# Kernel tuning notes

Measured on AMD Instinct MI355X. Metric: run time of the kernel, lower is better.

Reference implementation:

```python
import jax, jax.numpy as jnp
import numpy as np

GROUPS = 9  # hardcoded in GTLModuleV1.forward


def setup_inputs() -> dict:
    key = jax.random.key(0)
    k1, k2, k3 = jax.random.split(key, 3)
    B, C, N, K = 4, 144, 16384, 16
    queryandkey = jax.random.normal(k1, (B, C, N), dtype=jnp.float32)
    value = jax.random.normal(k2, (B, C, N), dtype=jnp.float32)
    idx_knn = jax.random.randint(k3, (B, N, K), 0, N, dtype=jnp.int32)
    return {"queryandkey": queryandkey, "value": value, "idx_knn": idx_knn}


def _gather_neighbours(x, idx_flat, B, G, d, N, K):
    # x: (B, G, d, N); idx_flat: (B, 1, 1, N*K) -> (B, G, d, N, K)
    g = jnp.take_along_axis(x, jnp.broadcast_to(idx_flat, (B, G, d, N * K)), axis=3)
    return g.reshape(B, G, d, N, K)


def reference(queryandkey, value, idx_knn):
    B, C, N = queryandkey.shape
    K = idx_knn.shape[-1]
    G = GROUPS
    d = C // G  # Cl = C (Cnl = 0 in GTLModuleV1)

    q = queryandkey.reshape(B, G, d, N)          # LocalQuery == LocalKey source
    v = value.reshape(B, G, d, N)
    idx_flat = idx_knn.reshape(B, 1, 1, N * K)

    key_g = _gather_neighbours(q, idx_flat, B, G, d, N, K)  # (B,G,d,N,K)
    val_g = _gather_neighbours(v, idx_flat, B, G, d, N, K)  # (B,G,d,N,K)

    # LocalAtt = sum_d Q * K_gathered, softmax over neighbors
    att = jnp.einsum('bgdn,bgdnk->bgnk', q, key_g)
    att = jax.nn.softmax(att, axis=-1)                       # (B,G,N,K)

    # attention centrality: scatter_add of attention weights onto neighbor ids
    cent = jnp.zeros((B, G, N), dtype=att.dtype).at[
        jnp.arange(B)[:, None, None, None],
        jnp.arange(G)[None, :, None, None],
        idx_knn[:, None, :, :],
    ].add(att)                                               # (B,G,N)

    # weighted aggregation of gathered values
    feat = jnp.einsum('bgnk,bgdnk->bgdn', att, val_g).reshape(B, C, N)
    return feat, cent
```

## Files before the change

### kernel.cpp

```cpp
#include <hip/hip_runtime.h>
#include <hip/hip_fp16.h>

#define BATCH 4
#define CHAN  144
#define NPTS  16384
#define KNN   16
#define GRP   9
#define DIM   16
#define ROWU2 160
#define PCHA  16
#define PCHB  32
#define NPAIR (BATCH * GRP)

#define TT 32

typedef __attribute__((ext_vector_type(2))) _Float16 h2v;
typedef __attribute__((ext_vector_type(4))) float    f4v;
typedef __attribute__((ext_vector_type(4))) int      i4v;
typedef __attribute__((ext_vector_type(4))) unsigned u4v;
__device__ __forceinline__ h2v as_h2(unsigned int u) {
  union { unsigned int u; h2v h; } c; c.u = u; return c.h;
}
__device__ __forceinline__ float2 h2f(unsigned u) {
  union { unsigned u; __half2 h; } c; c.u = u;
  return __half22float2(c.h);
}

template<int J>
__device__ __forceinline__ int ibcast(int v) {
  return __builtin_amdgcn_update_dpp(0, v, (J) * 0x55, 0xF, 0xF, true);
}
template<int C>
__device__ __forceinline__ float fxor(float x) {
  int r = __builtin_amdgcn_update_dpp(0, __builtin_bit_cast(int, x), C, 0xF, 0xF, true);
  return __builtin_bit_cast(float, r);
}

__global__ __launch_bounds__(256) void pack_qv_kernel(
    const float* __restrict__ q, const float* __restrict__ v,
    unsigned int* __restrict__ qvT) {
  __shared__ float tq[TT][TT + 1];
  __shared__ float tv[TT][TT + 1];
  const int b = blockIdx.z;
  const float* qb = q + (size_t)b * CHAN * NPTS;
  const float* vb = v + (size_t)b * CHAN * NPTS;
  unsigned int* out = qvT + (size_t)b * NPTS * ROWU2;
  const int n0 = blockIdx.x * TT;
  const int c0 = blockIdx.y * TT;
  const int t = threadIdx.x;

  {
    const int cl = t >> 3, nq = (t & 7) * 4;
    const int c = c0 + cl;
    if (c < CHAN) {
      const float4 a = *(const float4*)&qb[(size_t)c * NPTS + n0 + nq];
      tq[cl][nq + 0] = a.x; tq[cl][nq + 1] = a.y;
      tq[cl][nq + 2] = a.z; tq[cl][nq + 3] = a.w;
      const float4 w = *(const float4*)&vb[(size_t)c * NPTS + n0 + nq];
      tv[cl][nq + 0] = w.x; tv[cl][nq + 1] = w.y;
      tv[cl][nq + 2] = w.z; tv[cl][nq + 3] = w.w;
    }
  }
  __syncthreads();
  {
    const int nl = t >> 3, cq = (t & 7) * 4;
    const int c = c0 + cq;
    if (c < CHAN) {
      __half2 k01 = __halves2half2(__float2half_rn(tq[cq + 0][nl]),
                                   __float2half_rn(tq[cq + 1][nl]));
      __half2 v01 = __halves2half2(__float2half_rn(tv[cq + 0][nl]),
                                   __float2half_rn(tv[cq + 1][nl]));
      __half2 k23 = __halves2half2(__float2half_rn(tq[cq + 2][nl]),
                                   __float2half_rn(tq[cq + 3][nl]));
      __half2 v23 = __halves2half2(__float2half_rn(tv[cq + 2][nl]),
                                   __float2half_rn(tv[cq + 3][nl]));
      *(uint4*)&out[(size_t)(n0 + nl) * ROWU2 + c] =
          make_uint4(*(unsigned int*)&k01, *(unsigned int*)&v01,
                     *(unsigned int*)&k23, *(unsigned int*)&v23);
    }
  }
}

__global__ __launch_bounds__(512, 4) void gtl_pair_kernel(
    const unsigned int* __restrict__ qvT,
    const int*   __restrict__ idx,
    float* __restrict__ feat,
    float* __restrict__ partA)
{
  const int i = blockIdx.x;
  const int x = i & 7, sblk = i >> 3;
  const int PU = x + 8 * (sblk >> 4);
  const int chunk = sblk & 15;
  const int b = PU >> 2, j = PU & 3;

  extern __shared__ float lcent[];
  const int tid = threadIdx.x;

  f4v* l4 = (f4v*)lcent;
  #pragma unroll
  for (int ii = 0; ii < 2 * NPTS / 4 / 512; ++ii)
    l4[ii * 512 + tid] = (f4v){0.f, 0.f, 0.f, 0.f};
  __syncthreads();

  const int lane = tid & 63;
  const int wv   = tid >> 6;
  const int slot = lane >> 3;
  const int e    = lane & 7;
  const int gh   = e >> 2;
  const int d    = e & 3;

  const char* qvb  = (const char*)qvT + (size_t)b * NPTS * (ROWU2 * 4);
  const char* idxB = (const char*)idx + (size_t)b * NPTS * (KNN * 4);
  const unsigned laneB  = (unsigned)(j * 128 + e * 16);
  const unsigned idxoff = (unsigned)(d * 16);

  int n = chunk * 1024 + wv * 8 + slot;
  i4v idq; u4v qq;
  asm volatile("global_load_dwordx4 %0, %1, %2"
               : "=v"(idq) : "v"((unsigned)n * 64u + idxoff), "s"(idxB));
  asm volatile("global_load_dwordx4 %0, %1, %2"
               : "=v"(qq) : "v"((unsigned)n * (ROWU2 * 4u) + laneB), "s"(qvb));
  asm volatile("s_waitcnt vmcnt(0)" ::: "memory");
  __builtin_amdgcn_sched_barrier(0);

  for (int it = 0; it < 16; ++it) {
    const h2v q01 = as_h2(qq.x);
    const h2v q23 = as_h2(qq.z);

    u4v kvA[8], kvB[8];
#define GISS(DST, K)                                                         \
    {                                                                        \
      const int mk = ibcast<((K) >> 2)>(                                     \
          ((K) & 3) == 0 ? idq.x : ((K) & 3) == 1 ? idq.y                    \
                         : ((K) & 3) == 2 ? idq.z : idq.w);                  \
      const unsigned vo = (unsigned)mk * (ROWU2 * 4u) + laneB;               \
      asm volatile("global_load_dwordx4 %0, %1, %2"                          \
                   : "=v"(DST) : "v"(vo), "s"(qvb));                         \
    }
    GISS(kvA[0], 0)  GISS(kvA[1], 1)  GISS(kvA[2], 2)  GISS(kvA[3], 3)
    GISS(kvA[4], 4)  GISS(kvA[5], 5)  GISS(kvA[6], 6)  GISS(kvA[7], 7)
    GISS(kvB[0], 8)  GISS(kvB[1], 9)  GISS(kvB[2], 10) GISS(kvB[3], 11)
    GISS(kvB[4], 12) GISS(kvB[5], 13) GISS(kvB[6], 14) GISS(kvB[7], 15)
#undef GISS

    const int itn = (it + 1 < 16) ? it + 1 : it;
    const int nn = chunk * 1024 + itn * 64 + wv * 8 + slot;
    i4v idqn; u4v qqn;
    asm volatile("global_load_dwordx4 %0, %1, %2"
                 : "=v"(idqn) : "v"((unsigned)nn * 64u + idxoff), "s"(idxB));
    asm volatile("global_load_dwordx4 %0, %1, %2"
                 : "=v"(qqn) : "v"((unsigned)nn * (ROWU2 * 4u) + laneB), "s"(qvb));

    asm volatile("s_waitcnt vmcnt(10)" ::: "memory");
    __builtin_amdgcn_sched_barrier(0);

    float kp[4] = {0.f, 0.f, 0.f, 0.f};
    float sum = 0.f, a0 = 0.f, a1 = 0.f, a2 = 0.f, a3 = 0.f;
#define CSTEP(V, K)                                                          \
    {                                                                        \
      float s = __builtin_amdgcn_fdot2(as_h2((V).x), q01, 0.f, false);       \
      s = __builtin_amdgcn_fdot2(as_h2((V).z), q23, s, false);               \
      s += fxor<0xB1>(s);                                                    \
      s += fxor<0x4E>(s);                                                    \
      const float e2 = __expf(s);                                            \
      sum += e2;                                                             \
      kp[(K) & 3] = (d == ((K) >> 2)) ? e2 : kp[(K) & 3];                    \
      const float2 v01 = h2f((V).y);                                         \
      const float2 v23 = h2f((V).w);                                         \
      a0 += e2 * v01.x; a1 += e2 * v01.y; a2 += e2 * v23.x; a3 += e2 * v23.y;\
    }
    CSTEP(kvA[0], 0)  CSTEP(kvA[1], 1)  CSTEP(kvA[2], 2)  CSTEP(kvA[3], 3)
    CSTEP(kvA[4], 4)  CSTEP(kvA[5], 5)  CSTEP(kvA[6], 6)  CSTEP(kvA[7], 7)

    asm volatile("s_waitcnt vmcnt(2)" ::: "memory");
    __builtin_amdgcn_sched_barrier(0);
    CSTEP(kvB[0], 8)  CSTEP(kvB[1], 9)  CSTEP(kvB[2], 10) CSTEP(kvB[3], 11)
    CSTEP(kvB[4], 12) CSTEP(kvB[5], 13) CSTEP(kvB[6], 14) CSTEP(kvB[7], 15)
#undef CSTEP

    const float inv = 1.f / sum;

    float* lc = lcent + gh * NPTS;
    atomicAdd(&lc[idq.x], kp[0] * inv);
    atomicAdd(&lc[idq.y], kp[1] * inv);
    atomicAdd(&lc[idq.z], kp[2] * inv);
    atomicAdd(&lc[idq.w], kp[3] * inv);

    float* fb = feat + ((size_t)b * CHAN + (2 * j + gh) * DIM + 4 * d) * NPTS + n;
    __builtin_nontemporal_store(a0 * inv, fb);
    __builtin_nontemporal_store(a1 * inv, fb + NPTS);
    __builtin_nontemporal_store(a2 * inv, fb + 2 * NPTS);
    __builtin_nontemporal_store(a3 * inv, fb + 3 * NPTS);

    asm volatile("s_waitcnt vmcnt(4)" ::: "memory");
    __builtin_amdgcn_sched_barrier(0);
    n = nn; idq = idqn; qq = qqn;
  }
  asm volatile("s_waitcnt vmcnt(0)" ::: "memory");
  __builtin_amdgcn_sched_barrier(0);

  __syncthreads();
  f4v* p4 = (f4v*)(partA + ((size_t)(PU * PCHA + chunk) * 2) * NPTS);
  #pragma unroll
  for (int i2 = 0; i2 < 2 * NPTS / 4 / 512; ++i2) {
    const int j2 = (i2 * 512 + tid + chunk * 512) & 8191;
    __builtin_nontemporal_store(l4[j2], &p4[j2]);
  }
}

__global__ __launch_bounds__(512, 4) void gtl_g8_kernel(
    const unsigned int* __restrict__ qvT,
    const int*   __restrict__ idx,
    float* __restrict__ feat,
    float* __restrict__ partB)
{
  const int i = blockIdx.x;
  const int x = i & 7, sblk = i >> 3;
  const int b = x >> 1;
  const int chunk = sblk + 16 * (x & 1);

  __shared__ float lcent[NPTS];
  const int tid = threadIdx.x;
  f4v* l4 = (f4v*)lcent;
  #pragma unroll
  for (int ii = 0; ii < NPTS / 4 / 512; ++ii)
    l4[ii * 512 + tid] = (f4v){0.f, 0.f, 0.f, 0.f};
  __syncthreads();

  const int NG = 4;
  const int gstart = chunk * NG;

  const int lane = tid & 63;
  const int wv   = tid >> 6;
  const int slot = lane >> 2;
  const int d    = lane & 3;

  const char* qvb  = (const char*)qvT + (size_t)b * NPTS * (ROWU2 * 4);
  const char* idxB = (const char*)idx + (size_t)b * NPTS * (KNN * 4);
  const unsigned laneB  = (unsigned)(8 * 64 + d * 16);
  const unsigned idxoff = (unsigned)(d * 16);

  int n = gstart * 128 + wv * 16 + slot;
  i4v idq; u4v qq;
  asm volatile("global_load_dwordx4 %0, %1, %2"
               : "=v"(idq) : "v"((unsigned)n * 64u + idxoff), "s"(idxB));
  asm volatile("global_load_dwordx4 %0, %1, %2"
               : "=v"(qq) : "v"((unsigned)n * (ROWU2 * 4u) + laneB), "s"(qvb));
  asm volatile("s_waitcnt vmcnt(0)" ::: "memory");
  __builtin_amdgcn_sched_barrier(0);

  for (int it = 0; it < NG; ++it) {
    const h2v q01 = as_h2(qq.x);
    const h2v q23 = as_h2(qq.z);

    u4v kvA[8], kvB[8];
#define GISS(DST, K)                                                         \
    {                                                                        \
      const int mk = ibcast<((K) >> 2)>(                                     \
          ((K) & 3) == 0 ? idq.x : ((K) & 3) == 1 ? idq.y                    \
                         : ((K) & 3) == 2 ? idq.z : idq.w);                  \
      const unsigned vo = (unsigned)mk * (ROWU2 * 4u) + laneB;               \
      asm volatile("global_load_dwordx4 %0, %1, %2"                          \
                   : "=v"(DST) : "v"(vo), "s"(qvb));                         \
    }
    GISS(kvA[0], 0)  GISS(kvA[1], 1)  GISS(kvA[2], 2)  GISS(kvA[3], 3)
    GISS(kvA[4], 4)  GISS(kvA[5], 5)  GISS(kvA[6], 6)  GISS(kvA[7], 7)
    GISS(kvB[0], 8)  GISS(kvB[1], 9)  GISS(kvB[2], 10) GISS(kvB[3], 11)
    GISS(kvB[4], 12) GISS(kvB[5], 13) GISS(kvB[6], 14) GISS(kvB[7], 15)
#undef GISS

    const int itn = (it + 1 < NG) ? it + 1 : it;
    const int nn = (gstart + itn) * 128 + wv * 16 + slot;
    i4v idqn; u4v qqn;
    asm volatile("global_load_dwordx4 %0, %1, %2"
                 : "=v"(idqn) : "v"((unsigned)nn * 64u + idxoff), "s"(idxB));
    asm volatile("global_load_dwordx4 %0, %1, %2"
                 : "=v"(qqn) : "v"((unsigned)nn * (ROWU2 * 4u) + laneB), "s"(qvb));

    asm volatile("s_waitcnt vmcnt(10)" ::: "memory");
    __builtin_amdgcn_sched_barrier(0);

    float kp[4] = {0.f, 0.f, 0.f, 0.f};
    float sum = 0.f, a0 = 0.f, a1 = 0.f, a2 = 0.f, a3 = 0.f;
#define CSTEP(V, K)                                                          \
    {                                                                        \
      float s = __builtin_amdgcn_fdot2(as_h2((V).x), q01, 0.f, false);       \
      s = __builtin_amdgcn_fdot2(as_h2((V).z), q23, s, false);               \
      s += fxor<0xB1>(s);                                                    \
      s += fxor<0x4E>(s);                                                    \
      const float e2 = __expf(s);                                            \
      sum += e2;                                                             \
      kp[(K) & 3] = (d == ((K) >> 2)) ? e2 : kp[(K) & 3];                    \
      const float2 v01 = h2f((V).y);                                         \
      const float2 v23 = h2f((V).w);                                         \
      a0 += e2 * v01.x; a1 += e2 * v01.y; a2 += e2 * v23.x; a3 += e2 * v23.y;\
    }
    CSTEP(kvA[0], 0)  CSTEP(kvA[1], 1)  CSTEP(kvA[2], 2)  CSTEP(kvA[3], 3)
    CSTEP(kvA[4], 4)  CSTEP(kvA[5], 5)  CSTEP(kvA[6], 6)  CSTEP(kvA[7], 7)
    asm volatile("s_waitcnt vmcnt(2)" ::: "memory");
    __builtin_amdgcn_sched_barrier(0);
    CSTEP(kvB[0], 8)  CSTEP(kvB[1], 9)  CSTEP(kvB[2], 10) CSTEP(kvB[3], 11)
    CSTEP(kvB[4], 12) CSTEP(kvB[5], 13) CSTEP(kvB[6], 14) CSTEP(kvB[7], 15)
#undef CSTEP

    const float inv = 1.f / sum;
    atomicAdd(&lcent[idq.x], kp[0] * inv);
    atomicAdd(&lcent[idq.y], kp[1] * inv);
    atomicAdd(&lcent[idq.z], kp[2] * inv);
    atomicAdd(&lcent[idq.w], kp[3] * inv);

    float* fb = feat + ((size_t)b * CHAN + 8 * DIM + 4 * d) * NPTS + n;
    __builtin_nontemporal_store(a0 * inv, fb);
    __builtin_nontemporal_store(a1 * inv, fb + NPTS);
    __builtin_nontemporal_store(a2 * inv, fb + 2 * NPTS);
    __builtin_nontemporal_store(a3 * inv, fb + 3 * NPTS);

    asm volatile("s_waitcnt vmcnt(4)" ::: "memory");
    __builtin_amdgcn_sched_barrier(0);
    n = nn; idq = idqn; qq = qqn;
  }
  asm volatile("s_waitcnt vmcnt(0)" ::: "memory");
  __builtin_amdgcn_sched_barrier(0);

  __syncthreads();
  f4v* p4 = (f4v*)(partB + (size_t)(b * PCHB + chunk) * NPTS);
  #pragma unroll
  for (int i2 = 0; i2 < NPTS / 4 / 512; ++i2) {
    const int j2 = (i2 * 512 + tid + chunk * 128) & 4095;
    __builtin_nontemporal_store(l4[j2], &p4[j2]);
  }
}

__global__ __launch_bounds__(256) void reduce_cent_kernel(
    const float* __restrict__ partA, const float* __restrict__ partB,
    float* __restrict__ cent) {
  const int t = blockIdx.x * 256 + threadIdx.x;
  const int bg = t >> 12;
  const int m4 = (t & 4095) << 2;
  const int b = bg / GRP, g = bg - b * GRP;
  f4v s = (f4v){0.f, 0.f, 0.f, 0.f};
  if (g < 8) {
    const int PU = b * 4 + (g >> 1), gh = g & 1;
    const f4v* p = (const f4v*)(partA + ((size_t)(PU * PCHA) * 2 + gh) * NPTS + m4);
    #pragma unroll
    for (int i = 0; i < PCHA; ++i)
      s += __builtin_nontemporal_load(&p[(size_t)i * 2 * (NPTS / 4)]);
  } else {
    const f4v* p = (const f4v*)(partB + (size_t)(b * PCHB) * NPTS + m4);
    #pragma unroll
    for (int i = 0; i < PCHB; ++i)
      s += __builtin_nontemporal_load(&p[(size_t)i * (NPTS / 4)]);
  }
  *(f4v*)(cent + (size_t)bg * NPTS + m4) = s;
}

extern "C" void kernel_launch(void* const* d_in, const int* in_sizes, int n_in,
                              void* d_out, int out_size, void* d_ws, size_t ws_size,
                              hipStream_t stream) {
  const float* q   = (const float*)d_in[0];
  const float* v   = (const float*)d_in[1];
  const int*   idx = (const int*)d_in[2];

  float* feat = (float*)d_out;
  float* cent = feat + (size_t)BATCH * CHAN * NPTS;

  unsigned int* qvT = (unsigned int*)d_ws;
  float* partA = (float*)(qvT + (size_t)BATCH * NPTS * ROWU2);
  float* partB = partA + (size_t)16 * PCHA * 2 * NPTS;

  dim3 tg(NPTS / TT, (CHAN + TT - 1) / TT, BATCH);
  pack_qv_kernel<<<tg, 256, 0, stream>>>(q, v, qvT);

  gtl_pair_kernel<<<256, 512, 2 * NPTS * sizeof(float), stream>>>(
      qvT, idx, feat, partA);

  gtl_g8_kernel<<<128, 512, 0, stream>>>(qvT, idx, feat, partB);

  reduce_cent_kernel<<<(NPAIR * NPTS / 4) / 256, 256, 0, stream>>>(
      partA, partB, cent);
}
```

Before: 210.2 us.

## Fuse pair and group-8 attention kernels into one 1024-thread launch

Result: faster. 199.0 us (-5.3%).

```diff
diff --git a/kernel.cpp b/kernel.cpp
--- a/kernel.cpp
+++ b/kernel.cpp
@@ -9,7 +9,7 @@
 #define DIM   16
 #define ROWU2 160
 #define PCHA  16
-#define PCHB  32
+#define PCHB  64
 #define NPAIR (BATCH * GRP)
 
 #define TT 32
@@ -81,49 +81,163 @@
   }
 }
 
-__global__ __launch_bounds__(512, 4) void gtl_pair_kernel(
+__global__ __launch_bounds__(1024, 4) void gtl_fused_kernel(
     const unsigned int* __restrict__ qvT,
     const int*   __restrict__ idx,
     float* __restrict__ feat,
-    float* __restrict__ partA)
+    float* __restrict__ partA,
+    float* __restrict__ partB)
 {
+  extern __shared__ float lcent[];
   const int i = blockIdx.x;
-  const int x = i & 7, sblk = i >> 3;
-  const int PU = x + 8 * (sblk >> 4);
-  const int chunk = sblk & 15;
-  const int b = PU >> 2, j = PU & 3;
-
-  extern __shared__ float lcent[];
   const int tid = threadIdx.x;
-
   f4v* l4 = (f4v*)lcent;
-  #pragma unroll
-  for (int ii = 0; ii < 2 * NPTS / 4 / 512; ++ii)
-    l4[ii * 512 + tid] = (f4v){0.f, 0.f, 0.f, 0.f};
-  __syncthreads();
-
-  const int lane = tid & 63;
-  const int wv   = tid >> 6;
-  const int slot = lane >> 3;
-  const int e    = lane & 7;
-  const int gh   = e >> 2;
-  const int d    = e & 3;
-
-  const char* qvb  = (const char*)qvT + (size_t)b * NPTS * (ROWU2 * 4);
-  const char* idxB = (const char*)idx + (size_t)b * NPTS * (KNN * 4);
-  const unsigned laneB  = (unsigned)(j * 128 + e * 16);
-  const unsigned idxoff = (unsigned)(d * 16);
-
-  int n = chunk * 1024 + wv * 8 + slot;
-  i4v idq; u4v qq;
-  asm volatile("global_load_dwordx4 %0, %1, %2"
-               : "=v"(idq) : "v"((unsigned)n * 64u + idxoff), "s"(idxB));
-  asm volatile("global_load_dwordx4 %0, %1, %2"
-               : "=v"(qq) : "v"((unsigned)n * (ROWU2 * 4u) + laneB), "s"(qvb));
-  asm volatile("s_waitcnt vmcnt(0)" ::: "memory");
-  __builtin_amdgcn_sched_barrier(0);
-
-  for (int it = 0; it < 16; ++it) {
+
+  if (i < 256) {
+    const int x = i & 7, sblk = i >> 3;
+    const int PU = x + 8 * (sblk >> 4);
+    const int chunk = sblk & 15;
+    const int b = PU >> 2, j = PU & 3;
+
+    #pragma unroll
+    for (int ii = 0; ii < 2 * NPTS / 4 / 1024; ++ii)
+      l4[ii * 1024 + tid] = (f4v){0.f, 0.f, 0.f, 0.f};
+    __syncthreads();
+
+    const int lane = tid & 63;
+    const int wv   = tid >> 6;
+    const int slot = lane >> 3;
+    const int e    = lane & 7;
+    const int gh   = e >> 2;
+    const int d    = e & 3;
+
+    const char* qvb  = (const char*)qvT + (size_t)b * NPTS * (ROWU2 * 4);
+    const char* idxB = (const char*)idx + (size_t)b * NPTS * (KNN * 4);
+    const unsigned laneB  = (unsigned)(j * 128 + e * 16);
+    const unsigned idxoff = (unsigned)(d * 16);
+
+    int n = chunk * 1024 + wv * 8 + slot;
+    i4v idq; u4v qq;
+    asm volatile("global_load_dwordx4 %0, %1, %2"
+                 : "=v"(idq) : "v"((unsigned)n * 64u + idxoff), "s"(idxB));
+    asm volatile("global_load_dwordx4 %0, %1, %2"
+                 : "=v"(qq) : "v"((unsigned)n * (ROWU2 * 4u) + laneB), "s"(qvb));
+    asm volatile("s_waitcnt vmcnt(0)" ::: "memory");
+    __builtin_amdgcn_sched_barrier(0);
+
+    for (int it = 0; it < 8; ++it) {
+      const h2v q01 = as_h2(qq.x);
+      const h2v q23 = as_h2(qq.z);
+
+      u4v kvA[8], kvB[8];
+#define GISS(DST, K)                                                         \
+      {                                                                      \
+        const int mk = ibcast<((K) >> 2)>(                                   \
+            ((K) & 3) == 0 ? idq.x : ((K) & 3) == 1 ? idq.y                  \
+                           : ((K) & 3) == 2 ? idq.z : idq.w);                \
+        const unsigned vo = (unsigned)mk * (ROWU2 * 4u) + laneB;             \
+        asm volatile("global_load_dwordx4 %0, %1, %2"                        \
+                     : "=v"(DST) : "v"(vo), "s"(qvb));                       \
+      }
+      GISS(kvA[0], 0)  GISS(kvA[1], 1)  GISS(kvA[2], 2)  GISS(kvA[3], 3)
+      GISS(kvA[4], 4)  GISS(kvA[5], 5)  GISS(kvA[6], 6)  GISS(kvA[7], 7)
+      GISS(kvB[0], 8)  GISS(kvB[1], 9)  GISS(kvB[2], 10) GISS(kvB[3], 11)
+      GISS(kvB[4], 12) GISS(kvB[5], 13) GISS(kvB[6], 14) GISS(kvB[7], 15)
+#undef GISS
+
+      const int itn = (it + 1 < 8) ? it + 1 : it;
+      const int nn = chunk * 1024 + itn * 128 + wv * 8 + slot;
+      i4v idqn; u4v qqn;
+      asm volatile("global_load_dwordx4 %0, %1, %2"
+                   : "=v"(idqn) : "v"((unsigned)nn * 64u + idxoff), "s"(idxB));
+      asm volatile("global_load_dwordx4 %0, %1, %2"
+                   : "=v"(qqn) : "v"((unsigned)nn * (ROWU2 * 4u) + laneB), "s"(qvb));
+
+      asm volatile("s_waitcnt vmcnt(10)" ::: "memory");
+      __builtin_amdgcn_sched_barrier(0);
+
+      float kp[4] = {0.f, 0.f, 0.f, 0.f};
+      float sum = 0.f, a0 = 0.f, a1 = 0.f, a2 = 0.f, a3 = 0.f;
+#define CSTEP(V, K)                                                          \
+      {                                                                      \
+        float s = __builtin_amdgcn_fdot2(as_h2((V).x), q01, 0.f, false);     \
+        s = __builtin_amdgcn_fdot2(as_h2((V).z), q23, s, false);             \
+        s += fxor<0xB1>(s);                                                  \
+        s += fxor<0x4E>(s);                                                  \
+        const float e2 = __expf(s);                                          \
+        sum += e2;                                                           \
+        kp[(K) & 3] = (d == ((K) >> 2)) ? e2 : kp[(K) & 3];                  \
+        const float2 v01 = h2f((V).y);                                       \
+        const float2 v23 = h2f((V).w);                                       \
+        a0 += e2 * v01.x; a1 += e2 * v01.y;                                  \
+        a2 += e2 * v23.x; a3 += e2 * v23.y;                                  \
+      }
+      CSTEP(kvA[0], 0)  CSTEP(kvA[1], 1)  CSTEP(kvA[2], 2)  CSTEP(kvA[3], 3)
+      CSTEP(kvA[4], 4)  CSTEP(kvA[5], 5)  CSTEP(kvA[6], 6)  CSTEP(kvA[7], 7)
+
+      asm volatile("s_waitcnt vmcnt(2)" ::: "memory");
+      __builtin_amdgcn_sched_barrier(0);
+      CSTEP(kvB[0], 8)  CSTEP(kvB[1], 9)  CSTEP(kvB[2], 10) CSTEP(kvB[3], 11)
+      CSTEP(kvB[4], 12) CSTEP(kvB[5], 13) CSTEP(kvB[6], 14) CSTEP(kvB[7], 15)
+#undef CSTEP
+
+      const float inv = 1.f / sum;
+      float* lc = lcent + gh * NPTS;
+      atomicAdd(&lc[idq.x], kp[0] * inv);
+      atomicAdd(&lc[idq.y], kp[1] * inv);
+      atomicAdd(&lc[idq.z], kp[2] * inv);
+      atomicAdd(&lc[idq.w], kp[3] * inv);
+
+      float* fb = feat + ((size_t)b * CHAN + (2 * j + gh) * DIM + 4 * d) * NPTS + n;
+      __builtin_nontemporal_store(a0 * inv, fb);
+      __builtin_nontemporal_store(a1 * inv, fb + NPTS);
+      __builtin_nontemporal_store(a2 * inv, fb + 2 * NPTS);
+      __builtin_nontemporal_store(a3 * inv, fb + 3 * NPTS);
+
+      asm volatile("s_waitcnt vmcnt(4)" ::: "memory");
+      __builtin_amdgcn_sched_barrier(0);
+      n = nn; idq = idqn; qq = qqn;
+    }
+    asm volatile("s_waitcnt vmcnt(0)" ::: "memory");
+    __builtin_amdgcn_sched_barrier(0);
+
+    __syncthreads();
+    f4v* p4 = (f4v*)(partA + ((size_t)(PU * PCHA + chunk) * 2) * NPTS);
+    #pragma unroll
+    for (int i2 = 0; i2 < 2 * NPTS / 4 / 1024; ++i2) {
+      const int j2 = (i2 * 1024 + tid + chunk * 512) & 8191;
+      __builtin_nontemporal_store(l4[j2], &p4[j2]);
+    }
+  } else {
+    const int i2b = i - 256;
+    const int x = i2b & 7, s = i2b >> 3;
+    const int b = x >> 1;
+    const int chunk = s + 32 * (x & 1);
+
+    #pragma unroll
+    for (int ii = 0; ii < NPTS / 4 / 1024; ++ii)
+      l4[ii * 1024 + tid] = (f4v){0.f, 0.f, 0.f, 0.f};
+    __syncthreads();
+
+    const int lane = tid & 63;
+    const int wv   = tid >> 6;
+    const int slot = lane >> 2;
+    const int d    = lane & 3;
+
+    const char* qvb  = (const char*)qvT + (size_t)b * NPTS * (ROWU2 * 4);
+    const char* idxB = (const char*)idx + (size_t)b * NPTS * (KNN * 4);
+    const unsigned laneB  = (unsigned)(8 * 64 + d * 16);
+    const unsigned idxoff = (unsigned)(d * 16);
+
+    const int n = chunk * 256 + wv * 16 + slot;
+    i4v idq; u4v qq;
+    asm volatile("global_load_dwordx4 %0, %1, %2"
+                 : "=v"(idq) : "v"((unsigned)n * 64u + idxoff), "s"(idxB));
+    asm volatile("global_load_dwordx4 %0, %1, %2"
+                 : "=v"(qq) : "v"((unsigned)n * (ROWU2 * 4u) + laneB), "s"(qvb));
+    asm volatile("s_waitcnt vmcnt(0)" ::: "memory");
+    __builtin_amdgcn_sched_barrier(0);
+
     const h2v q01 = as_h2(qq.x);
     const h2v q23 = as_h2(qq.z);
 
@@ -143,161 +257,28 @@
     GISS(kvB[4], 12) GISS(kvB[5], 13) GISS(kvB[6], 14) GISS(kvB[7], 15)
 #undef GISS
 
-    const int itn = (it + 1 < 16) ? it + 1 : it;
-    const int nn = chunk * 1024 + itn * 64 + wv * 8 + slot;
-    i4v idqn; u4v qqn;
-    asm volatile("global_load_dwordx4 %0, %1, %2"
-                 : "=v"(idqn) : "v"((unsigned)nn * 64u + idxoff), "s"(idxB));
-    asm volatile("global_load_dwordx4 %0, %1, %2"
-                 : "=v"(qqn) : "v"((unsigned)nn * (ROWU2 * 4u) + laneB), "s"(qvb));
-
-    asm volatile("s_waitcnt vmcnt(10)" ::: "memory");
+    asm volatile("s_waitcnt vmcnt(8)" ::: "memory");
     __builtin_amdgcn_sched_barrier(0);
 
     float kp[4] = {0.f, 0.f, 0.f, 0.f};
     float sum = 0.f, a0 = 0.f, a1 = 0.f, a2 = 0.f, a3 = 0.f;
 #define CSTEP(V, K)                                                          \
     {                                                                        \
-      float s = __builtin_amdgcn_fdot2(as_h2((V).x), q01, 0.f, false);       \
-      s = __builtin_amdgcn_fdot2(as_h2((V).z), q23, s, false);               \
-      s += fxor<0xB1>(s);                                                    \
-      s += fxor<0x4E>(s);                                                    \
-      const float e2 = __expf(s);                                            \
+      float sc = __builtin_amdgcn_fdot2(as_h2((V).x), q01, 0.f, false);      \
+      sc = __builtin_amdgcn_fdot2(as_h2((V).z), q23, sc, false);             \
+      sc += fxor<0xB1>(sc);                                                  \
+      sc += fxor<0x4E>(sc);                                                  \
+      const float e2 = __expf(sc);                                           \
       sum += e2;                                                             \
       kp[(K) & 3] = (d == ((K) >> 2)) ? e2 : kp[(K) & 3];                    \
       const float2 v01 = h2f((V).y);                                         \
       const float2 v23 = h2f((V).w);                                         \
-      a0 += e2 * v01.x; a1 += e2 * v01.y; a2 += e2 * v23.x; a3 += e2 * v23.y;\
+      a0 += e2 * v01.x; a1 += e2 * v01.y;                                    \
+      a2 += e2 * v23.x; a3 += e2 * v23.y;                                    \
     }
     CSTEP(kvA[0], 0)  CSTEP(kvA[1], 1)  CSTEP(kvA[2], 2)  CSTEP(kvA[3], 3)
     CSTEP(kvA[4], 4)  CSTEP(kvA[5], 5)  CSTEP(kvA[6], 6)  CSTEP(kvA[7], 7)
-
-    asm volatile("s_waitcnt vmcnt(2)" ::: "memory");
-    __builtin_amdgcn_sched_barrier(0);
-    CSTEP(kvB[0], 8)  CSTEP(kvB[1], 9)  CSTEP(kvB[2], 10) CSTEP(kvB[3], 11)
-    CSTEP(kvB[4], 12) CSTEP(kvB[5], 13) CSTEP(kvB[6], 14) CSTEP(kvB[7], 15)
-#undef CSTEP
-
-    const float inv = 1.f / sum;
-
-    float* lc = lcent + gh * NPTS;
-    atomicAdd(&lc[idq.x], kp[0] * inv);
-    atomicAdd(&lc[idq.y], kp[1] * inv);
-    atomicAdd(&lc[idq.z], kp[2] * inv);
-    atomicAdd(&lc[idq.w], kp[3] * inv);
-
-    float* fb = feat + ((size_t)b * CHAN + (2 * j + gh) * DIM + 4 * d) * NPTS + n;
-    __builtin_nontemporal_store(a0 * inv, fb);
-    __builtin_nontemporal_store(a1 * inv, fb + NPTS);
-    __builtin_nontemporal_store(a2 * inv, fb + 2 * NPTS);
-    __builtin_nontemporal_store(a3 * inv, fb + 3 * NPTS);
-
-    asm volatile("s_waitcnt vmcnt(4)" ::: "memory");
-    __builtin_amdgcn_sched_barrier(0);
-    n = nn; idq = idqn; qq = qqn;
-  }
-  asm volatile("s_waitcnt vmcnt(0)" ::: "memory");
-  __builtin_amdgcn_sched_barrier(0);
-
-  __syncthreads();
-  f4v* p4 = (f4v*)(partA + ((size_t)(PU * PCHA + chunk) * 2) * NPTS);
-  #pragma unroll
-  for (int i2 = 0; i2 < 2 * NPTS / 4 / 512; ++i2) {
-    const int j2 = (i2 * 512 + tid + chunk * 512) & 8191;
-    __builtin_nontemporal_store(l4[j2], &p4[j2]);
-  }
-}
-
-__global__ __launch_bounds__(512, 4) void gtl_g8_kernel(
-    const unsigned int* __restrict__ qvT,
-    const int*   __restrict__ idx,
-    float* __restrict__ feat,
-    float* __restrict__ partB)
-{
-  const int i = blockIdx.x;
-  const int x = i & 7, sblk = i >> 3;
-  const int b = x >> 1;
-  const int chunk = sblk + 16 * (x & 1);
-
-  __shared__ float lcent[NPTS];
-  const int tid = threadIdx.x;
-  f4v* l4 = (f4v*)lcent;
-  #pragma unroll
-  for (int ii = 0; ii < NPTS / 4 / 512; ++ii)
-    l4[ii * 512 + tid] = (f4v){0.f, 0.f, 0.f, 0.f};
-  __syncthreads();
-
-  const int NG = 4;
-  const int gstart = chunk * NG;
-
-  const int lane = tid & 63;
-  const int wv   = tid >> 6;
-  const int slot = lane >> 2;
-  const int d    = lane & 3;
-
-  const char* qvb  = (const char*)qvT + (size_t)b * NPTS * (ROWU2 * 4);
-  const char* idxB = (const char*)idx + (size_t)b * NPTS * (KNN * 4);
-  const unsigned laneB  = (unsigned)(8 * 64 + d * 16);
-  const unsigned idxoff = (unsigned)(d * 16);
-
-  int n = gstart * 128 + wv * 16 + slot;
-  i4v idq; u4v qq;
-  asm volatile("global_load_dwordx4 %0, %1, %2"
-               : "=v"(idq) : "v"((unsigned)n * 64u + idxoff), "s"(idxB));
-  asm volatile("global_load_dwordx4 %0, %1, %2"
-               : "=v"(qq) : "v"((unsigned)n * (ROWU2 * 4u) + laneB), "s"(qvb));
-  asm volatile("s_waitcnt vmcnt(0)" ::: "memory");
-  __builtin_amdgcn_sched_barrier(0);
-
-  for (int it = 0; it < NG; ++it) {
-    const h2v q01 = as_h2(qq.x);
-    const h2v q23 = as_h2(qq.z);
-
-    u4v kvA[8], kvB[8];
-#define GISS(DST, K)                                                         \
-    {                                                                        \
-      const int mk = ibcast<((K) >> 2)>(                                     \
-          ((K) & 3) == 0 ? idq.x : ((K) & 3) == 1 ? idq.y                    \
-                         : ((K) & 3) == 2 ? idq.z : idq.w);                  \
-      const unsigned vo = (unsigned)mk * (ROWU2 * 4u) + laneB;               \
-      asm volatile("global_load_dwordx4 %0, %1, %2"                          \
-                   : "=v"(DST) : "v"(vo), "s"(qvb));                         \
-    }
-    GISS(kvA[0], 0)  GISS(kvA[1], 1)  GISS(kvA[2], 2)  GISS(kvA[3], 3)
-    GISS(kvA[4], 4)  GISS(kvA[5], 5)  GISS(kvA[6], 6)  GISS(kvA[7], 7)
-    GISS(kvB[0], 8)  GISS(kvB[1], 9)  GISS(kvB[2], 10) GISS(kvB[3], 11)
-    GISS(kvB[4], 12) GISS(kvB[5], 13) GISS(kvB[6], 14) GISS(kvB[7], 15)
-#undef GISS
-
-    const int itn = (it + 1 < NG) ? it + 1 : it;
-    const int nn = (gstart + itn) * 128 + wv * 16 + slot;
-    i4v idqn; u4v qqn;
-    asm volatile("global_load_dwordx4 %0, %1, %2"
-                 : "=v"(idqn) : "v"((unsigned)nn * 64u + idxoff), "s"(idxB));
-    asm volatile("global_load_dwordx4 %0, %1, %2"
-                 : "=v"(qqn) : "v"((unsigned)nn * (ROWU2 * 4u) + laneB), "s"(qvb));
-
-    asm volatile("s_waitcnt vmcnt(10)" ::: "memory");
-    __builtin_amdgcn_sched_barrier(0);
-
-    float kp[4] = {0.f, 0.f, 0.f, 0.f};
-    float sum = 0.f, a0 = 0.f, a1 = 0.f, a2 = 0.f, a3 = 0.f;
-#define CSTEP(V, K)                                                          \
-    {                                                                        \
-      float s = __builtin_amdgcn_fdot2(as_h2((V).x), q01, 0.f, false);       \
-      s = __builtin_amdgcn_fdot2(as_h2((V).z), q23, s, false);               \
-      s += fxor<0xB1>(s);                                                    \
-      s += fxor<0x4E>(s);                                                    \
-      const float e2 = __expf(s);                                            \
-      sum += e2;                                                             \
-      kp[(K) & 3] = (d == ((K) >> 2)) ? e2 : kp[(K) & 3];                    \
-      const float2 v01 = h2f((V).y);                                         \
-      const float2 v23 = h2f((V).w);                                         \
-      a0 += e2 * v01.x; a1 += e2 * v01.y; a2 += e2 * v23.x; a3 += e2 * v23.y;\
-    }
-    CSTEP(kvA[0], 0)  CSTEP(kvA[1], 1)  CSTEP(kvA[2], 2)  CSTEP(kvA[3], 3)
-    CSTEP(kvA[4], 4)  CSTEP(kvA[5], 5)  CSTEP(kvA[6], 6)  CSTEP(kvA[7], 7)
-    asm volatile("s_waitcnt vmcnt(2)" ::: "memory");
+    asm volatile("s_waitcnt vmcnt(0)" ::: "memory");
     __builtin_amdgcn_sched_barrier(0);
     CSTEP(kvB[0], 8)  CSTEP(kvB[1], 9)  CSTEP(kvB[2], 10) CSTEP(kvB[3], 11)
     CSTEP(kvB[4], 12) CSTEP(kvB[5], 13) CSTEP(kvB[6], 14) CSTEP(kvB[7], 15)
@@ -315,19 +296,13 @@
     __builtin_nontemporal_store(a2 * inv, fb + 2 * NPTS);
     __builtin_nontemporal_store(a3 * inv, fb + 3 * NPTS);
 
-    asm volatile("s_waitcnt vmcnt(4)" ::: "memory");
-    __builtin_amdgcn_sched_barrier(0);
-    n = nn; idq = idqn; qq = qqn;
-  }
-  asm volatile("s_waitcnt vmcnt(0)" ::: "memory");
-  __builtin_amdgcn_sched_barrier(0);
-
-  __syncthreads();
-  f4v* p4 = (f4v*)(partB + (size_t)(b * PCHB + chunk) * NPTS);
-  #pragma unroll
-  for (int i2 = 0; i2 < NPTS / 4 / 512; ++i2) {
-    const int j2 = (i2 * 512 + tid + chunk * 128) & 4095;
-    __builtin_nontemporal_store(l4[j2], &p4[j2]);
+    __syncthreads();
+    f4v* p4 = (f4v*)(partB + (size_t)(b * PCHB + chunk) * NPTS);
+    #pragma unroll
+    for (int i2 = 0; i2 < NPTS / 4 / 1024; ++i2) {
+      const int j2 = (i2 * 1024 + tid + chunk * 64) & 4095;
+      __builtin_nontemporal_store(l4[j2], &p4[j2]);
+    }
   }
 }
 
@@ -371,10 +346,8 @@
   dim3 tg(NPTS / TT, (CHAN + TT - 1) / TT, BATCH);
   pack_qv_kernel<<<tg, 256, 0, stream>>>(q, v, qvT);
 
-  gtl_pair_kernel<<<256, 512, 2 * NPTS * sizeof(float), stream>>>(
-      qvT, idx, feat, partA);
-
-  gtl_g8_kernel<<<128, 512, 0, stream>>>(qvT, idx, feat, partB);
+  gtl_fused_kernel<<<512, 1024, 2 * NPTS * sizeof(float), stream>>>(
+      qvT, idx, feat, partA, partB);
 
   reduce_cent_kernel<<<(NPAIR * NPTS / 4) / 256, 256, 0, stream>>>(
       partA, partB, cent);
```
